# Kernel optimization log

Measured on AMD Instinct MI355X. Metric: run time of the kernel, lower is better.

Reference implementation:

```python
import jax, jax.numpy as jnp
import numpy as np

B, S, DIM, HEADS, HD, FF = 2, 2048, 1024, 16, 64, 4096
PREV, MAX_SEQ, THETA, POS_BIAS_MAX, EPS = 1024, 4096, 10000.0, 2.0, 1e-6


def _freqs_cos_sin():
    inv = 1.0 / THETA ** (np.arange(0, HD, 2)[: HD // 2].astype(np.float32) / HD)
    f = np.outer(np.arange(MAX_SEQ, dtype=np.float32), inv)
    return jnp.asarray(np.cos(f), jnp.float32), jnp.asarray(np.sin(f), jnp.float32)


def setup_inputs():
    key = jax.random.key(0)
    ks = jax.random.split(key, 16)
    lin = lambda k, o, i: 0.02 * jax.random.normal(k, (o, i), jnp.float32)
    cos, sin = _freqs_cos_sin()
    return {
        "x": jax.random.normal(ks[0], (B, S, DIM), jnp.float32),
        "cache_k": jax.random.normal(ks[1], (B, HEADS, PREV, HD), jnp.float32),
        "cache_v": jax.random.normal(ks[2], (B, HEADS, PREV, HD), jnp.float32),
        "cos": cos, "sin": sin,
        "attn_norm_w": jnp.ones((DIM,), jnp.float32),
        "ffn_norm_w": jnp.ones((DIM,), jnp.float32),
        "wq": lin(ks[3], DIM, DIM), "bq": jnp.zeros((DIM,), jnp.float32),
        "wk": lin(ks[4], DIM, DIM), "bk": jnp.zeros((DIM,), jnp.float32),
        "wv": lin(ks[5], DIM, DIM), "bv": jnp.zeros((DIM,), jnp.float32),
        "wo": lin(ks[6], DIM, DIM), "bo": jnp.zeros((DIM,), jnp.float32),
        "w_gate": lin(ks[7], FF, DIM), "b_gate": jnp.zeros((FF,), jnp.float32),
        "w_value": lin(ks[8], FF, DIM), "b_value": jnp.zeros((FF,), jnp.float32),
        "w_proj": lin(ks[9], DIM, FF), "b_proj": jnp.zeros((DIM,), jnp.float32),
        "cache_limit": 3072,
    }


def _rmsnorm(h, w):
    return h * jax.lax.rsqrt(jnp.mean(h * h, axis=-1, keepdims=True) + EPS) * w


def _rope(t, cos, sin):
    # t: [B,H,L,HD]; cos/sin: [L, HD//2]; rotate interleaved pairs (complex mult)
    t2 = t.reshape(t.shape[:-1] + (HD // 2, 2))
    x0, x1 = t2[..., 0], t2[..., 1]
    c = cos[None, None]
    s = sin[None, None]
    out = jnp.stack([x0 * c - x1 * s, x0 * s + x1 * c], axis=-1)
    return out.reshape(t.shape)


def _forward(x, cache_k, cache_v, cos, sin, attn_norm_w, ffn_norm_w, wq, bq, wk, bk, wv, bv, wo, bo, w_gate, b_gate, w_value, b_value, w_proj, b_proj, cache_limit):
    b, s, d = x.shape
    h = _rmsnorm(x, attn_norm_w)
    shape4 = lambda t: t.reshape(b, s, HEADS, HD).transpose(0, 2, 1, 3)  # [B,H,S,HD]
    q = shape4(h @ wq.T + bq)
    k_new = shape4(h @ wk.T + bk)
    v_new = shape4(h @ wv.T + bv)
    k_all = jnp.concatenate([cache_k, k_new], axis=2)
    v_all = jnp.concatenate([cache_v, v_new], axis=2)
    if cache_limit > 0:
        k_all = k_all[:, :, -cache_limit:, :]
        v_all = v_all[:, :, -cache_limit:, :]
    total = k_all.shape[2]
    prev = total - s
    # RoPE: q at absolute positions prev..prev+s-1, keys at 0..total-1 (mod cache len)
    pos_q = (jnp.arange(s) + prev) % MAX_SEQ
    pos_k = jnp.arange(total) % MAX_SEQ
    q = _rope(q, cos[pos_q], sin[pos_q])
    k = _rope(k_all, cos[pos_k], sin[pos_k])
    # linear positional bias + causal mask over the new-token block only
    slope = POS_BIAS_MAX / max(total - 1, 1)
    j = jnp.arange(total, dtype=jnp.float32)[None, :]
    i_abs = (prev + jnp.arange(s, dtype=jnp.float32))[:, None]
    bias = slope * (j - i_abs)  # [s, total]
    causal = (jnp.arange(total)[None, :] - prev) > jnp.arange(s)[:, None]
    mask = jnp.where(causal, -jnp.inf, bias)
    scores = jnp.einsum('bhsd,bhtd->bhst', q, k) / jnp.sqrt(jnp.float32(HD)) + mask
    attn = jax.nn.softmax(scores, axis=-1)
    ctx = jnp.einsum('bhst,bhtd->bhsd', attn, v_all)
    ctx = ctx.transpose(0, 2, 1, 3).reshape(b, s, d)
    x = x + ctx @ wo.T + bo
    h2 = _rmsnorm(x, ffn_norm_w)
    gated = jax.nn.silu(h2 @ w_gate.T + b_gate) * (h2 @ w_value.T + b_value)
    return x + gated @ w_proj.T + b_proj


def reference(x, cache_k, cache_v, cos, sin, attn_norm_w, ffn_norm_w, wq, bq, wk, bk, wv, bv, wo, bo, w_gate, b_gate, w_value, b_value, w_proj, b_proj, cache_limit):
    return _forward(x, cache_k, cache_v, cos, sin, attn_norm_w, ffn_norm_w, wq, bq, wk, bk, wv, bv, wo, bo, w_gate, b_gate, w_value, b_value, w_proj, b_proj, cache_limit)
```

## Files before the change

### kernel.cpp

```cpp
#include <hip/hip_runtime.h>
#include <stdint.h>

typedef unsigned short u16;
typedef unsigned int   u32;
typedef __bf16 bf16x8 __attribute__((ext_vector_type(8)));
typedef float  f32x4  __attribute__((ext_vector_type(4)));
typedef u32    u32x4  __attribute__((ext_vector_type(4)));
typedef u32    u32x2  __attribute__((ext_vector_type(2)));

#define B_SZ  2
#define S_LEN 2048
#define NH    16
#define HD    64
#define DIM   1024
#define FF    4096
#define T_LEN 3072
#define PREV  1024
#define MROWS (B_SZ * S_LEN)
#define LOG2E 1.44269504f

#define MFMA16 __builtin_amdgcn_mfma_f32_16x16x32_bf16

__device__ __forceinline__ u16 f2bf(float f) {
  u32 u = __builtin_bit_cast(u32, f);
  u32 r = u + 0x7FFFu + ((u >> 16) & 1u);
  return (u16)(r >> 16);
}
__device__ __forceinline__ float bf2f(u16 h) {
  u32 u = ((u32)h) << 16;
  return __builtin_bit_cast(float, u);
}
__device__ __forceinline__ u32 cvtpk(float lo, float hi) {
  u32 r;
  asm("v_cvt_pk_bf16_f32 %0, %1, %2" : "=v"(r) : "v"(lo), "v"(hi));
  return r;
}

__device__ __forceinline__ void gl_lds16(const void* g, void* l) {
  __builtin_amdgcn_global_load_lds(
      (const __attribute__((address_space(1))) u32*)g,
      (__attribute__((address_space(3))) u32*)l, 16, 0, 0);
}

#define GFENCE() asm volatile("" ::: "memory")
#define BARF()                         \
  do {                                 \
    GFENCE();                          \
    __builtin_amdgcn_s_barrier();      \
    GFENCE();                          \
  } while (0)

__global__ __launch_bounds__(256) void cvt_kernel(const float* __restrict__ src,
                                                  u16* __restrict__ dst, int n4) {
  int i = blockIdx.x * 256 + threadIdx.x;
  const int stride = gridDim.x * 256;
  for (; i < n4; i += stride) {
    f32x4 v = *(const f32x4*)&src[(long)i * 4];
    u32x2 o;
    o[0] = (u32)f2bf(v[0]) | ((u32)f2bf(v[1]) << 16);
    o[1] = (u32)f2bf(v[2]) | ((u32)f2bf(v[3]) << 16);
    *(u32x2*)&dst[(long)i * 4] = o;
  }
}

__global__ __launch_bounds__(256) void cvt_sw_kernel(const float* __restrict__ src,
                                                     u16* __restrict__ dst, int nunits) {
  int i = blockIdx.x * 256 + threadIdx.x;
  const int stride = gridDim.x * 256;
  for (; i < nunits; i += stride) {
    int row = i >> 7;
    int g = i & 127;
    const float* s = &src[((long)row << 10) + g * 8];
    f32x4 a = *(const f32x4*)s;
    f32x4 b = *(const f32x4*)(s + 4);
    u32x4 o;
    o[0] = (u32)f2bf(a[0]) | ((u32)f2bf(a[1]) << 16);
    o[1] = (u32)f2bf(a[2]) | ((u32)f2bf(a[3]) << 16);
    o[2] = (u32)f2bf(b[0]) | ((u32)f2bf(b[1]) << 16);
    o[3] = (u32)f2bf(b[2]) | ((u32)f2bf(b[3]) << 16);
    const int gp = (g & ~7) | ((g & 7) ^ (row & 7));
    *(u32x4*)&dst[((long)row << 10) + gp * 8] = o;
  }
}

__global__ __launch_bounds__(256) void cvt_ilv_sw_kernel(const float* __restrict__ wg,
                                                         const float* __restrict__ wval,
                                                         u16* __restrict__ dst) {
  int i = blockIdx.x * 256 + threadIdx.x;
  const int stride = gridDim.x * 256;
  for (; i < FF * 128; i += stride) {
    int j = i >> 7;
    int g = i & 127;
    const float* sg = &wg[((long)j << 10) + g * 8];
    const float* sv = &wval[((long)j << 10) + g * 8];
    f32x4 a = *(const f32x4*)sg;
    f32x4 b = *(const f32x4*)(sg + 4);
    u32x4 og;
    og[0] = (u32)f2bf(a[0]) | ((u32)f2bf(a[1]) << 16);
    og[1] = (u32)f2bf(a[2]) | ((u32)f2bf(a[3]) << 16);
    og[2] = (u32)f2bf(b[0]) | ((u32)f2bf(b[1]) << 16);
    og[3] = (u32)f2bf(b[2]) | ((u32)f2bf(b[3]) << 16);
    f32x4 c = *(const f32x4*)sv;
    f32x4 d = *(const f32x4*)(sv + 4);
    u32x4 ov;
    ov[0] = (u32)f2bf(c[0]) | ((u32)f2bf(c[1]) << 16);
    ov[1] = (u32)f2bf(c[2]) | ((u32)f2bf(c[3]) << 16);
    ov[2] = (u32)f2bf(d[0]) | ((u32)f2bf(d[1]) << 16);
    ov[3] = (u32)f2bf(d[2]) | ((u32)f2bf(d[3]) << 16);
    const int rg = 2 * j, rv = 2 * j + 1;
    const int gpg = (g & ~7) | ((g & 7) ^ (rg & 7));
    const int gpv = (g & ~7) | ((g & 7) ^ (rv & 7));
    *(u32x4*)&dst[((long)rg << 10) + gpg * 8] = og;
    *(u32x4*)&dst[((long)rv << 10) + gpv * 8] = ov;
  }
}

__global__ __launch_bounds__(256) void bias_ilv_kernel(const float* __restrict__ bg,
                                                       const float* __restrict__ bval,
                                                       float* __restrict__ dst) {
  int i = blockIdx.x * 256 + threadIdx.x;
  if (i < FF) {
    dst[2 * i] = bg[i];
    dst[2 * i + 1] = bval[i];
  }
}

__global__ __launch_bounds__(256) void rmsnorm_kernel(const float* __restrict__ x,
                                                      const float* __restrict__ w,
                                                      u16* __restrict__ out) {
  const int row = blockIdx.x;
  const int tid = threadIdx.x;
  const long base = (long)row * DIM + tid * 4;
  f32x4 v = *(const f32x4*)&x[base];
  float ss = v[0] * v[0] + v[1] * v[1] + v[2] * v[2] + v[3] * v[3];
#pragma unroll
  for (int d = 1; d <= 32; d <<= 1) ss += __shfl_xor(ss, d, 64);
  __shared__ float red[4];
  if ((tid & 63) == 0) red[tid >> 6] = ss;
  __syncthreads();
  float tot = red[0] + red[1] + red[2] + red[3];
  const float sc = rsqrtf(tot * (1.f / (float)DIM) + 1e-6f);
  f32x4 wv4 = *(const f32x4*)&w[tid * 4];
  u32x2 o;
  o[0] = (u32)f2bf(v[0] * sc * wv4[0]) | ((u32)f2bf(v[1] * sc * wv4[1]) << 16);
  o[1] = (u32)f2bf(v[2] * sc * wv4[2]) | ((u32)f2bf(v[3] * sc * wv4[3]) << 16);
  const int u = tid >> 1, hf = tid & 1;
  const int up = (u & 0x78) | ((u & 7) ^ (row & 7));
  *(u32x2*)&out[(long)row * DIM + up * 8 + hf * 4] = o;
}

template <int EPI>
__global__ __launch_bounds__(512, 2) void gemm256(const u16* __restrict__ A,
                                                  const u16* __restrict__ Bw,
                                                  const float* __restrict__ bias,
                                                  u16* __restrict__ out_bf,
                                                  int N, int K) {
  __shared__ __align__(16) u16 Ab[2][256 * 64];
  __shared__ __align__(16) u16 Bb[2][256 * 64];
  const int tid = threadIdx.x;
  const int lane = tid & 63;
  const int wid = tid >> 6;
  const int wm = wid >> 2, wn = wid & 3;
  const int l15 = lane & 15, lhi = lane >> 4;
  const int c7 = l15 & 7;
  const long m0 = (long)blockIdx.y * 256;
  const long n0 = (long)blockIdx.x * 256;
  const int NT = K >> 6;

  const int srow = tid >> 3;
  const int sunit = (tid & 7) * 8;
  const u16* agp = A + (m0 + srow) * K + sunit;
  const u16* bgp = Bw + (n0 + srow) * K + sunit;
  const int ldst = tid * 8;

  auto stageA = [&](int kt, int b) {
    const int k0 = kt << 6;
    u16* d = &Ab[b][0];
#pragma unroll
    for (int c = 0; c < 4; ++c)
      gl_lds16(agp + (long)(c * 64) * K + k0, d + c * 4096 + ldst);
  };
  auto stageB = [&](int kt, int b) {
    const int k0 = kt << 6;
    u16* d = &Bb[b][0];
#pragma unroll
    for (int c = 0; c < 4; ++c)
      gl_lds16(bgp + (long)(c * 64) * K + k0, d + c * 4096 + ldst);
  };

#define READ_A(MH)                                                               \
  _Pragma("unroll") for (int m_ = 0; m_ < 4; ++m_) {                             \
    _Pragma("unroll") for (int ks_ = 0; ks_ < 2; ++ks_) {                        \
      Afr[MH][m_ * 2 + ks_] =                                                    \
          *(const bf16x8*)&Ac[(wm * 128 + (MH)*64 + m_ * 16 + l15) * 64 +        \
                              (((ks_ * 4 + lhi) ^ c7) * 8)];                     \
    }                                                                            \
  }
#define READ_B(NH)                                                               \
  _Pragma("unroll") for (int n_ = 0; n_ < 2; ++n_) {                             \
    _Pragma("unroll") for (int ks_ = 0; ks_ < 2; ++ks_) {                        \
      Bfr[NH][n_ * 2 + ks_] =                                                    \
          *(const bf16x8*)&Bc[(wn * 64 + (NH)*32 + n_ * 16 + l15) * 64 +         \
                              (((ks_ * 4 + lhi) ^ c7) * 8)];                     \
    }                                                                            \
  }
#define QUAD(MH, NH)                                                             \
  do {                                                                           \
    __builtin_amdgcn_s_setprio(1);                                               \
    _Pragma("unroll") for (int m_ = 0; m_ < 4; ++m_) {                           \
      _Pragma("unroll") for (int n_ = 0; n_ < 2; ++n_) {                         \
        acc[(MH)*4 + m_][(NH)*2 + n_] =                                          \
            MFMA16(Afr[MH][m_ * 2], Bfr[NH][n_ * 2],                             \
                   acc[(MH)*4 + m_][(NH)*2 + n_], 0, 0, 0);                      \
        acc[(MH)*4 + m_][(NH)*2 + n_] =                                          \
            MFMA16(Afr[MH][m_ * 2 + 1], Bfr[NH][n_ * 2 + 1],                     \
                   acc[(MH)*4 + m_][(NH)*2 + n_], 0, 0, 0);                      \
      }                                                                          \
    }                                                                            \
    __builtin_amdgcn_s_setprio(0);                                               \
  } while (0)

  f32x4 acc[8][4] = {};

  stageA(0, 0);
  stageB(0, 0);
  stageA(1, 1);
  stageB(1, 1);
  asm volatile("s_waitcnt vmcnt(8)" ::: "memory");
  __builtin_amdgcn_s_barrier();
  GFENCE();

  for (int kt = 0; kt < NT; ++kt) {
    const int b = kt & 1;
    const u16* Ac = &Ab[b][0];
    const u16* Bc = &Bb[b][0];
    bf16x8 Afr[2][8], Bfr[2][4];
    READ_A(0);
    READ_B(0);
    BARF();
    QUAD(0, 0);
    BARF();
    READ_A(1);
    READ_B(1);
    BARF();
    QUAD(0, 1);
    BARF();
    if (kt + 2 < NT) stageA(kt + 2, b);
    BARF();
    QUAD(1, 0);
    BARF();
    if (kt + 2 < NT) stageB(kt + 2, b);
    BARF();
    QUAD(1, 1);
    if (kt + 1 < NT) {
      if (kt + 2 < NT)
        asm volatile("s_waitcnt vmcnt(8)" ::: "memory");
      else
        asm volatile("s_waitcnt vmcnt(0)" ::: "memory");
      __builtin_amdgcn_s_barrier();
      GFENCE();
    }
  }
#undef READ_A
#undef READ_B
#undef QUAD

#pragma unroll
  for (int mi = 0; mi < 8; ++mi) {
    const long row0 = m0 + wm * 128 + mi * 16 + lhi * 4;
#pragma unroll
    for (int ni = 0; ni < 4; ++ni) {
      const long col = n0 + wn * 64 + ni * 16 + l15;
      const float bb = bias[col];
#pragma unroll
      for (int r = 0; r < 4; ++r) {
        float v = acc[mi][ni][r] + bb;
        if (EPI == 2) {
          float other = __shfl_xor(v, 1, 64);
          if (!(l15 & 1)) {
            float s = v / (1.f + __expf(-v)) * other;
            out_bf[(row0 + r) * (N >> 1) + (col >> 1)] = f2bf(s);
          }
        } else {
          out_bf[(row0 + r) * N + col] = f2bf(v);
        }
      }
    }
  }
}

template <int EPI, int NB>
__global__ __launch_bounds__(256) void gemm_bt(const u16* __restrict__ A,
                                               const u16* __restrict__ Bw,
                                               const float* __restrict__ bias,
                                               const float* __restrict__ resid,
                                               u16* __restrict__ out_bf,
                                               float* __restrict__ out_f,
                                               int N, int K) {
  constexpr int BHALF = NB / 64;
  constexpr int NFR = NB / 32;
  constexpr int LPT = 2 + BHALF;
  __shared__ __align__(16) u16 As[3][128 * 32];
  __shared__ __align__(16) u16 Bs[3][NB * 32];
  const int tid = threadIdx.x;
  const int lane = tid & 63;
  const int wv = tid >> 6;
  const int wr = wv >> 1, wc = wv & 1;
  const long m0 = (long)blockIdx.y * 128;
  const long n0 = (long)blockIdx.x * NB;

  const int arow = tid >> 2;
  const int acol = (tid & 3) << 3;
  const u16* ag = A + (m0 + arow) * K + acol;
  const u16* bg = Bw + (n0 + arow) * K + acol;
  const long hK = (long)64 * K;

  f32x4 acc[4][NFR] = {};
  const int l15 = lane & 15;
  const int lhi = lane >> 4;
  const int aoff0 = (wr * 64 + l15) * 32 + lhi * 8;
  const int boff0 = (wc * (NB / 2) + l15) * 32 + lhi * 8;
  const int nk = K >> 5;

  auto stage = [&](int t, int buf) {
    const int k0 = t << 5;
    gl_lds16(ag + k0, &As[buf][tid * 8]);
    gl_lds16(ag + k0 + hK, &As[buf][2048 + tid * 8]);
    gl_lds16(bg + k0, &Bs[buf][tid * 8]);
    if (BHALF == 2) gl_lds16(bg + k0 + hK, &Bs[buf][2048 + tid * 8]);
  };

  stage(0, 0);
  stage(1, 1);
  asm volatile("s_waitcnt vmcnt(%0)" ::"n"(LPT) : "memory");
  __builtin_amdgcn_s_barrier();
  GFENCE();

  for (int t = 0; t < nk; ++t) {
    const int cb = t % 3;
    if (t + 2 < nk) stage(t + 2, (t + 2) % 3);
    bf16x8 af[4], bfr[NFR];
#pragma unroll
    for (int i = 0; i < 4; ++i) af[i] = *(const bf16x8*)&As[cb][aoff0 + i * 16 * 32];
#pragma unroll
    for (int j = 0; j < NFR; ++j) bfr[j] = *(const bf16x8*)&Bs[cb][boff0 + j * 16 * 32];
    __builtin_amdgcn_s_setprio(1);
#pragma unroll
    for (int i = 0; i < 4; ++i)
#pragma unroll
      for (int j = 0; j < NFR; ++j)
        acc[i][j] = MFMA16(af[i], bfr[j], acc[i][j], 0, 0, 0);
    __builtin_amdgcn_s_setprio(0);
    if (t + 2 < nk) {
      asm volatile("s_waitcnt vmcnt(%0)" ::"n"(LPT) : "memory");
      __builtin_amdgcn_s_barrier();
      GFENCE();
    } else if (t + 1 < nk) {
      asm volatile("s_waitcnt vmcnt(0)" ::: "memory");
      __builtin_amdgcn_s_barrier();
      GFENCE();
    }
  }

#pragma unroll
  for (int i = 0; i < 4; ++i) {
    const long row0 = m0 + wr * 64 + i * 16 + lhi * 4;
#pragma unroll
    for (int j = 0; j < NFR; ++j) {
      const long col = n0 + wc * (NB / 2) + j * 16 + l15;
      const float bb = bias[col];
#pragma unroll
      for (int r = 0; r < 4; ++r) {
        const long idx = (row0 + r) * N + col;
        float v = acc[i][j][r] + bb;
        if (EPI == 0) out_bf[idx] = f2bf(v);
        else          out_f[idx] = resid[idx] + v;
      }
    }
  }
}

__global__ __launch_bounds__(256) void rope_q_kernel(const u16* __restrict__ qkv,
                                                     const float* __restrict__ cosT,
                                                     const float* __restrict__ sinT,
                                                     u16* __restrict__ Q) {
  int idx = blockIdx.x * 256 + threadIdx.x;
  int u = idx & 7;
  int s = (idx >> 3) & (S_LEN - 1);
  int bh = idx >> 14;
  int b = bh >> 4, h = bh & 15;
  int pos = PREV + s;
  const float SC = 0.125f * LOG2E;
  const u16* src = qkv + ((long)(b * S_LEN + s)) * (3 * DIM) + h * HD + u * 8;
  u32x4 d = *(const u32x4*)src;
  f32x4 cv = *(const f32x4*)&cosT[(long)pos * 32 + u * 4];
  f32x4 sv = *(const f32x4*)&sinT[(long)pos * 32 + u * 4];
  u32x4 o;
#pragma unroll
  for (int p = 0; p < 4; ++p) {
    float x0 = bf2f((u16)(d[p] & 0xffff));
    float x1 = bf2f((u16)(d[p] >> 16));
    float y0 = (x0 * cv[p] - x1 * sv[p]) * SC;
    float y1 = (x0 * sv[p] + x1 * cv[p]) * SC;
    o[p] = (u32)f2bf(y0) | ((u32)f2bf(y1) << 16);
  }
  *(u32x4*)&Q[((long)bh * S_LEN + s) * HD + u * 8] = o;
}

__global__ __launch_bounds__(256) void rope_k_kernel(const u16* __restrict__ qkv,
                                                     const float* __restrict__ cache_k,
                                                     const float* __restrict__ cosT,
                                                     const float* __restrict__ sinT,
                                                     u16* __restrict__ Kall) {
  int idx = blockIdx.x * 256 + threadIdx.x;
  int u = idx & 7;
  int t2 = idx >> 3;
  int j = t2 % T_LEN;
  int bh = t2 / T_LEN;
  int b = bh >> 4, h = bh & 15;
  float e[8];
  if (j < PREV) {
    const float* src = cache_k + ((long)bh * PREV + j) * HD + u * 8;
    f32x4 a = *(const f32x4*)src;
    f32x4 c = *(const f32x4*)(src + 4);
    e[0] = a[0]; e[1] = a[1]; e[2] = a[2]; e[3] = a[3];
    e[4] = c[0]; e[5] = c[1]; e[6] = c[2]; e[7] = c[3];
  } else {
    const u16* src = qkv + ((long)(b * S_LEN + (j - PREV))) * (3 * DIM) + DIM + h * HD + u * 8;
    u32x4 d = *(const u32x4*)src;
#pragma unroll
    for (int p = 0; p < 4; ++p) {
      e[2 * p] = bf2f((u16)(d[p] & 0xffff));
      e[2 * p + 1] = bf2f((u16)(d[p] >> 16));
    }
  }
  f32x4 cv = *(const f32x4*)&cosT[(long)j * 32 + u * 4];
  f32x4 sv = *(const f32x4*)&sinT[(long)j * 32 + u * 4];
  u32x4 o;
#pragma unroll
  for (int p = 0; p < 4; ++p) {
    float y0 = e[2 * p] * cv[p] - e[2 * p + 1] * sv[p];
    float y1 = e[2 * p] * sv[p] + e[2 * p + 1] * cv[p];
    o[p] = (u32)f2bf(y0) | ((u32)f2bf(y1) << 16);
  }
  *(u32x4*)&Kall[((long)bh * T_LEN + j) * HD + (u ^ (j & 7)) * 8] = o;
}

__global__ __launch_bounds__(256) void build_vt_kernel(const u16* __restrict__ qkv,
                                                       const float* __restrict__ cache_v,
                                                       u16* __restrict__ Vtg) {
  int idx = blockIdx.x * 256 + threadIdx.x;
  int hd = idx & 63;
  int t2 = idx >> 6;
  int kb = t2 % 384;
  int bh = t2 / 384;
  int b = bh >> 4, h = bh & 15;
  int key0 = kb * 8;
  u16 vals[8];
  if (key0 < PREV) {
#pragma unroll
    for (int i = 0; i < 8; ++i)
      vals[i] = f2bf(cache_v[((long)bh * PREV + key0 + i) * HD + hd]);
  } else {
#pragma unroll
    for (int i = 0; i < 8; ++i)
      vals[i] = qkv[((long)(b * S_LEN + key0 + i - PREV)) * (3 * DIM) + 2 * DIM + h * HD + hd];
  }
  u32x4 o;
#pragma unroll
  for (int p = 0; p < 4; ++p)
    o[p] = (u32)vals[2 * p] | ((u32)vals[2 * p + 1] << 16);
  const int span = kb >> 3;
  const int u = (kb & 7) ^ (hd & 7);
  *(u32x4*)&Vtg[((long)bh * HD + hd) * T_LEN + span * 64 + u * 8] = o;
}

__global__ __launch_bounds__(256, 4) void attn_kernel(const u16* __restrict__ Q,
                                                      const u16* __restrict__ Kg,
                                                      const u16* __restrict__ Vtg,
                                                      u16* __restrict__ ctx, float slope2) {
  __shared__ __align__(16) u16 Ks[2][64 * 64];
  __shared__ __align__(16) u16 Vs[2][64 * 64];
  __shared__ __align__(16) u16 Ps[4][16 * 64];

  const int tid = threadIdx.x;
  const int lane = tid & 63;
  const int wv = tid >> 6;
  const int l15 = lane & 15;
  const int lhi = lane >> 4;
  const int c7 = l15 & 7;
  const int bh = blockIdx.x;
  const int qt = blockIdx.y;
  const int b = bh >> 4, h = bh & 15;
  const int q0 = qt * 64;
  const int nt = (PREV + q0 + 64) >> 6;

  const long qrow = (long)bh * S_LEN + q0 + wv * 16 + l15;
  bf16x8 aq0 = *(const bf16x8*)&Q[qrow * HD + lhi * 8];
  bf16x8 aq1 = *(const bf16x8*)&Q[qrow * HD + 32 + lhi * 8];

  const long kgb = (long)bh * T_LEN * HD;
  const long vgb = (long)bh * HD * T_LEN;
  const int srow = tid >> 3;
  const int sunit = (tid & 7) * 8;

  const u16* kst = Kg + kgb + (long)srow * HD + sunit;
  const u16* vst = Vtg + vgb + (long)srow * T_LEN + sunit;

  gl_lds16(kst, &Ks[0][tid * 8]);
  gl_lds16(kst + 32 * HD, &Ks[0][2048 + tid * 8]);
  gl_lds16(vst, &Vs[0][tid * 8]);
  gl_lds16(vst + (long)32 * T_LEN, &Vs[0][2048 + tid * 8]);
  kst += 64 * HD;
  vst += 64;
  __syncthreads();

  f32x4 o[4] = {};
  f32x4 lrun = {0.f, 0.f, 0.f, 0.f};
  float mrun = -1e30f;
  const int qq = wv * 16 + l15;
  u16* Pw = &Ps[wv][0];

  f32x4 be[4];
#pragma unroll
  for (int jf = 0; jf < 4; ++jf)
#pragma unroll
    for (int r = 0; r < 4; ++r)
      be[jf][r] = slope2 * (float)(jf * 16 + 4 * lhi + r);
  const float bmax = slope2 * 63.f;

  bf16x8 vones;
#pragma unroll
  for (int e = 0; e < 8; ++e) vones[e] = (__bf16)1.0f;

  float ktf = 0.f;
  const float kstep = slope2 * 64.f;

  for (int t = 0; t < nt; ++t) {
    const int cur = t & 1, nxt = cur ^ 1;
    const bool last = (t == nt - 1);
    if (!last) {
      gl_lds16(kst, &Ks[nxt][tid * 8]);
      gl_lds16(kst + 32 * HD, &Ks[nxt][2048 + tid * 8]);
      gl_lds16(vst, &Vs[nxt][tid * 8]);
      gl_lds16(vst + (long)32 * T_LEN, &Vs[nxt][2048 + tid * 8]);
      kst += 64 * HD;
      vst += 64;
    }

    f32x4 sf[4];
    __builtin_amdgcn_s_setprio(1);
#pragma unroll
    for (int jf = 0; jf < 4; ++jf) {
      const int krow = jf * 16 + l15;
      bf16x8 ak0 = *(const bf16x8*)&Ks[cur][krow * 64 + ((lhi ^ c7) * 8)];
      bf16x8 ak1 = *(const bf16x8*)&Ks[cur][krow * 64 + (((4 + lhi) ^ c7) * 8)];
      f32x4 s = {};
      s = MFMA16(ak0, aq0, s, 0, 0, 0);
      s = MFMA16(ak1, aq1, s, 0, 0, 0);
      sf[jf] = s;
    }
    __builtin_amdgcn_s_setprio(0);

    if (last) {
#pragma unroll
      for (int jf = 0; jf < 4; ++jf)
#pragma unroll
        for (int r = 0; r < 4; ++r)
          if (jf * 16 + 4 * lhi + r > qq) sf[jf][r] = -1e30f;
    }

    float h0 = fmaxf(fmaxf(sf[0][0], sf[0][1]), fmaxf(sf[0][2], sf[0][3]));
    float h1 = fmaxf(fmaxf(sf[1][0], sf[1][1]), fmaxf(sf[1][2], sf[1][3]));
    float h2 = fmaxf(fmaxf(sf[2][0], sf[2][1]), fmaxf(sf[2][2], sf[2][3]));
    float h3 = fmaxf(fmaxf(sf[3][0], sf[3][1]), fmaxf(sf[3][2], sf[3][3]));
    float pm = fmaxf(fmaxf(h0, h1), fmaxf(h2, h3));
    pm = fmaxf(pm, __shfl_xor(pm, 16, 64));
    pm = fmaxf(pm, __shfl_xor(pm, 32, 64));
    const float pmax_abs = pm + ktf + bmax;

    if (!__all(pmax_abs - mrun <= 8.f)) {
      const float mnew = fmaxf(mrun, pmax_abs);
      const float scl = exp2f(mrun - mnew);
      mrun = mnew;
#pragma unroll
      for (int r = 0; r < 4; ++r) {
        const float sr = __shfl(scl, 4 * lhi + r, 64);
        lrun[r] *= sr;
#pragma unroll
        for (int hf = 0; hf < 4; ++hf) o[hf][r] *= sr;
      }
    }
    const float meff = mrun - ktf;

#pragma unroll
    for (int jf = 0; jf < 4; ++jf) {
      f32x4 p;
#pragma unroll
      for (int r = 0; r < 4; ++r)
        p[r] = exp2f(sf[jf][r] + (be[jf][r] - meff));
      u32x2 pw2;
      pw2[0] = cvtpk(p[0], p[1]);
      pw2[1] = cvtpk(p[2], p[3]);
      const int u = (2 * jf + (lhi >> 1)) ^ c7;
      *(u32x2*)&Pw[l15 * 64 + u * 8 + (lhi & 1) * 4] = pw2;
    }

    bf16x8 pa0 = *(const bf16x8*)&Pw[l15 * 64 + ((lhi ^ c7) * 8)];
    bf16x8 pa1 = *(const bf16x8*)&Pw[l15 * 64 + (((4 + lhi) ^ c7) * 8)];
    f32x4 psum = {};
    __builtin_amdgcn_s_setprio(1);
    psum = MFMA16(pa0, vones, psum, 0, 0, 0);
    psum = MFMA16(pa1, vones, psum, 0, 0, 0);
#pragma unroll
    for (int hf = 0; hf < 4; ++hf) {
      const int vrow = hf * 16 + l15;
      bf16x8 bv0 = *(const bf16x8*)&Vs[cur][vrow * 64 + ((lhi ^ c7) * 8)];
      bf16x8 bv1 = *(const bf16x8*)&Vs[cur][vrow * 64 + (((4 + lhi) ^ c7) * 8)];
      o[hf] = MFMA16(pa0, bv0, o[hf], 0, 0, 0);
      o[hf] = MFMA16(pa1, bv1, o[hf], 0, 0, 0);
    }
    __builtin_amdgcn_s_setprio(0);
    lrun += psum;

    ktf += kstep;
    if (!last) __syncthreads();
  }

#pragma unroll
  for (int r = 0; r < 4; ++r) {
    const float inv = 1.f / lrun[r];
    const long srow_ = (long)b * S_LEN + q0 + wv * 16 + 4 * lhi + r;
#pragma unroll
    for (int hf = 0; hf < 4; ++hf)
      ctx[srow_ * DIM + h * HD + hf * 16 + l15] = f2bf(o[hf][r] * inv);
  }
}

extern "C" void kernel_launch(void* const* d_in, const int* in_sizes, int n_in,
                              void* d_out, int out_size, void* d_ws, size_t ws_size,
                              hipStream_t stream) {
  (void)in_sizes; (void)n_in; (void)out_size; (void)ws_size;
  const float* x       = (const float*)d_in[0];
  const float* cache_k = (const float*)d_in[1];
  const float* cache_v = (const float*)d_in[2];
  const float* cosT    = (const float*)d_in[3];
  const float* sinT    = (const float*)d_in[4];
  const float* attn_w  = (const float*)d_in[5];
  const float* ffn_w   = (const float*)d_in[6];
  const float* wq      = (const float*)d_in[7];
  const float* bq      = (const float*)d_in[8];
  const float* wk      = (const float*)d_in[9];
  const float* bk      = (const float*)d_in[10];
  const float* wv_     = (const float*)d_in[11];
  const float* bv      = (const float*)d_in[12];
  const float* wo      = (const float*)d_in[13];
  const float* bo      = (const float*)d_in[14];
  const float* wg      = (const float*)d_in[15];
  const float* bg      = (const float*)d_in[16];
  const float* wval    = (const float*)d_in[17];
  const float* bval    = (const float*)d_in[18];
  const float* wp      = (const float*)d_in[19];
  const float* bp      = (const float*)d_in[20];
  float* out = (float*)d_out;

  char* w = (char*)d_ws;
  size_t off = 0;
  auto alloc = [&](size_t bytes) -> char* {
    char* p = w + off;
    off += (bytes + 255) & ~(size_t)255;
    return p;
  };
  u16*   wqkv_bf  = (u16*)alloc((size_t)3 * DIM * DIM * 2);
  u16*   wo_bf    = (u16*)alloc((size_t)DIM * DIM * 2);
  u16*   wgv_bf   = (u16*)alloc((size_t)2 * FF * DIM * 2);
  u16*   wproj_bf = (u16*)alloc((size_t)DIM * FF * 2);
  float* bqkv     = (float*)alloc((size_t)3 * DIM * 4);
  float* bgv      = (float*)alloc((size_t)2 * FF * 4);
  float* x2       = (float*)alloc((size_t)MROWS * DIM * 4);
  char* AR = alloc((size_t)117440512);
  u16* qkv   = (u16*)(AR + 0);
  u16* Qb    = (u16*)(AR + 25165824);
  u16* Kb    = (u16*)(AR + 33554432);
  u16* Vtg   = (u16*)(AR + 46137344);
  u16* h1    = (u16*)(AR + 58720256);
  u16* ctx   = (u16*)(AR + 0);
  u16* h2    = (u16*)(AR + 8388608);
  u16* gated = (u16*)(AR + 16777216);

  cvt_sw_kernel<<<512, 256, 0, stream>>>(wq, wqkv_bf, DIM * DIM / 8);
  cvt_sw_kernel<<<512, 256, 0, stream>>>(wk, wqkv_bf + DIM * DIM, DIM * DIM / 8);
  cvt_sw_kernel<<<512, 256, 0, stream>>>(wv_, wqkv_bf + 2 * DIM * DIM, DIM * DIM / 8);
  cvt_kernel<<<512, 256, 0, stream>>>(wo, wo_bf, DIM * DIM / 4);
  cvt_ilv_sw_kernel<<<1024, 256, 0, stream>>>(wg, wval, wgv_bf);
  cvt_kernel<<<1024, 256, 0, stream>>>(wp, wproj_bf, DIM * FF / 4);
  bias_ilv_kernel<<<16, 256, 0, stream>>>(bg, bval, bgv);
  hipMemcpyAsync(bqkv, bq, DIM * 4, hipMemcpyDeviceToDevice, stream);
  hipMemcpyAsync(bqkv + DIM, bk, DIM * 4, hipMemcpyDeviceToDevice, stream);
  hipMemcpyAsync(bqkv + 2 * DIM, bv, DIM * 4, hipMemcpyDeviceToDevice, stream);

  rmsnorm_kernel<<<MROWS, 256, 0, stream>>>(x, attn_w, h1);
  gemm256<0><<<dim3(12, 16), 512, 0, stream>>>(h1, wqkv_bf, bqkv, qkv, 3 * DIM, DIM);
  rope_q_kernel<<<2048, 256, 0, stream>>>(qkv, cosT, sinT, Qb);
  rope_k_kernel<<<3072, 256, 0, stream>>>(qkv, cache_k, cosT, sinT, Kb);
  build_vt_kernel<<<3072, 256, 0, stream>>>(qkv, cache_v, Vtg);
  attn_kernel<<<dim3(B_SZ * NH, S_LEN / 64), 256, 0, stream>>>(
      Qb, Kb, Vtg, ctx, (2.0f / (float)(T_LEN - 1)) * LOG2E);
  gemm_bt<1, 64><<<dim3(16, 32), 256, 0, stream>>>(ctx, wo_bf, bo, x, nullptr, x2,
                                                   DIM, DIM);
  rmsnorm_kernel<<<MROWS, 256, 0, stream>>>(x2, ffn_w, h2);
  gemm256<2><<<dim3(32, 16), 512, 0, stream>>>(h2, wgv_bf, bgv, gated, 2 * FF, DIM);
  gemm_bt<1, 64><<<dim3(16, 32), 256, 0, stream>>>(gated, wproj_bf, bp, x2, nullptr, out,
                                                   DIM, FF);
}
```

Measured before the change: 383.2 us.

## Pair causal query tiles per block to balance work and share K/V loads

Each attention block now handles two query tiles, p and 31-p, so every block walks a similar number of key tiles under the causal mask. The short tile reuses the K and V tiles already staged in shared memory for the long one, which halves the grid and cuts redundant K/V traffic. The kernel keeps two sets of accumulators and preloads the V fragments into registers, so launch bounds drop to two blocks per SM. That costs occupancy and adds register pressure, and only 512 blocks are launched.

Result: faster. 372.6 us (-2.8%).

```diff
diff --git a/kernel.cpp b/kernel.cpp
--- a/kernel.cpp
+++ b/kernel.cpp
@@ -475,7 +475,7 @@
   *(u32x4*)&Vtg[((long)bh * HD + hd) * T_LEN + span * 64 + u * 8] = o;
 }
 
-__global__ __launch_bounds__(256, 4) void attn_kernel(const u16* __restrict__ Q,
+__global__ __launch_bounds__(256, 2) void attn_kernel(const u16* __restrict__ Q,
                                                       const u16* __restrict__ Kg,
                                                       const u16* __restrict__ Vtg,
                                                       u16* __restrict__ ctx, float slope2) {
@@ -490,14 +490,19 @@
   const int lhi = lane >> 4;
   const int c7 = l15 & 7;
   const int bh = blockIdx.x;
-  const int qt = blockIdx.y;
+  const int p = blockIdx.y;
   const int b = bh >> 4, h = bh & 15;
-  const int q0 = qt * 64;
-  const int nt = (PREV + q0 + 64) >> 6;
-
-  const long qrow = (long)bh * S_LEN + q0 + wv * 16 + l15;
-  bf16x8 aq0 = *(const bf16x8*)&Q[qrow * HD + lhi * 8];
-  bf16x8 aq1 = *(const bf16x8*)&Q[qrow * HD + 32 + lhi * 8];
+  const int qA0 = p * 64;
+  const int qB0 = (31 - p) * 64;
+  const int ntA = 17 + p;
+  const int ntB = 48 - p;
+
+  const long qrowA = (long)bh * S_LEN + qA0 + wv * 16 + l15;
+  const long qrowB = (long)bh * S_LEN + qB0 + wv * 16 + l15;
+  bf16x8 aqA0 = *(const bf16x8*)&Q[qrowA * HD + lhi * 8];
+  bf16x8 aqA1 = *(const bf16x8*)&Q[qrowA * HD + 32 + lhi * 8];
+  bf16x8 aqB0 = *(const bf16x8*)&Q[qrowB * HD + lhi * 8];
+  bf16x8 aqB1 = *(const bf16x8*)&Q[qrowB * HD + 32 + lhi * 8];
 
   const long kgb = (long)bh * T_LEN * HD;
   const long vgb = (long)bh * HD * T_LEN;
@@ -515,9 +520,9 @@
   vst += 64;
   __syncthreads();
 
-  f32x4 o[4] = {};
-  f32x4 lrun = {0.f, 0.f, 0.f, 0.f};
-  float mrun = -1e30f;
+  f32x4 oA[4] = {}, oB[4] = {};
+  f32x4 lrunA = {0.f, 0.f, 0.f, 0.f}, lrunB = {0.f, 0.f, 0.f, 0.f};
+  float mrunA = -1e30f, mrunB = -1e30f;
   const int qq = wv * 16 + l15;
   u16* Pw = &Ps[wv][0];
 
@@ -536,40 +541,15 @@
   float ktf = 0.f;
   const float kstep = slope2 * 64.f;
 
-  for (int t = 0; t < nt; ++t) {
-    const int cur = t & 1, nxt = cur ^ 1;
-    const bool last = (t == nt - 1);
-    if (!last) {
-      gl_lds16(kst, &Ks[nxt][tid * 8]);
-      gl_lds16(kst + 32 * HD, &Ks[nxt][2048 + tid * 8]);
-      gl_lds16(vst, &Vs[nxt][tid * 8]);
-      gl_lds16(vst + (long)32 * T_LEN, &Vs[nxt][2048 + tid * 8]);
-      kst += 64 * HD;
-      vst += 64;
-    }
-
-    f32x4 sf[4];
-    __builtin_amdgcn_s_setprio(1);
-#pragma unroll
-    for (int jf = 0; jf < 4; ++jf) {
-      const int krow = jf * 16 + l15;
-      bf16x8 ak0 = *(const bf16x8*)&Ks[cur][krow * 64 + ((lhi ^ c7) * 8)];
-      bf16x8 ak1 = *(const bf16x8*)&Ks[cur][krow * 64 + (((4 + lhi) ^ c7) * 8)];
-      f32x4 s = {};
-      s = MFMA16(ak0, aq0, s, 0, 0, 0);
-      s = MFMA16(ak1, aq1, s, 0, 0, 0);
-      sf[jf] = s;
-    }
-    __builtin_amdgcn_s_setprio(0);
-
-    if (last) {
+  auto process = [&](f32x4 (&sf)[4], bool maskNow, f32x4 (&o)[4], f32x4& lrun,
+                     float& mrun, bf16x8 (&vf)[8]) {
+    if (maskNow) {
 #pragma unroll
       for (int jf = 0; jf < 4; ++jf)
 #pragma unroll
         for (int r = 0; r < 4; ++r)
           if (jf * 16 + 4 * lhi + r > qq) sf[jf][r] = -1e30f;
     }
-
     float h0 = fmaxf(fmaxf(sf[0][0], sf[0][1]), fmaxf(sf[0][2], sf[0][3]));
     float h1 = fmaxf(fmaxf(sf[1][0], sf[1][1]), fmaxf(sf[1][2], sf[1][3]));
     float h2 = fmaxf(fmaxf(sf[2][0], sf[2][1]), fmaxf(sf[2][2], sf[2][3]));
@@ -595,13 +575,13 @@
 
 #pragma unroll
     for (int jf = 0; jf < 4; ++jf) {
-      f32x4 p;
+      f32x4 pp;
 #pragma unroll
       for (int r = 0; r < 4; ++r)
-        p[r] = exp2f(sf[jf][r] + (be[jf][r] - meff));
+        pp[r] = exp2f(sf[jf][r] + (be[jf][r] - meff));
       u32x2 pw2;
-      pw2[0] = cvtpk(p[0], p[1]);
-      pw2[1] = cvtpk(p[2], p[3]);
+      pw2[0] = cvtpk(pp[0], pp[1]);
+      pw2[1] = cvtpk(pp[2], pp[3]);
       const int u = (2 * jf + (lhi >> 1)) ^ c7;
       *(u32x2*)&Pw[l15 * 64 + u * 8 + (lhi & 1) * 4] = pw2;
     }
@@ -614,26 +594,81 @@
     psum = MFMA16(pa1, vones, psum, 0, 0, 0);
 #pragma unroll
     for (int hf = 0; hf < 4; ++hf) {
-      const int vrow = hf * 16 + l15;
-      bf16x8 bv0 = *(const bf16x8*)&Vs[cur][vrow * 64 + ((lhi ^ c7) * 8)];
-      bf16x8 bv1 = *(const bf16x8*)&Vs[cur][vrow * 64 + (((4 + lhi) ^ c7) * 8)];
-      o[hf] = MFMA16(pa0, bv0, o[hf], 0, 0, 0);
-      o[hf] = MFMA16(pa1, bv1, o[hf], 0, 0, 0);
+      o[hf] = MFMA16(pa0, vf[2 * hf], o[hf], 0, 0, 0);
+      o[hf] = MFMA16(pa1, vf[2 * hf + 1], o[hf], 0, 0, 0);
     }
     __builtin_amdgcn_s_setprio(0);
     lrun += psum;
+  };
+
+  for (int t = 0; t < ntB; ++t) {
+    const int cur = t & 1, nxt = cur ^ 1;
+    const bool lastStage = (t + 1 == ntB);
+    if (!lastStage) {
+      gl_lds16(kst, &Ks[nxt][tid * 8]);
+      gl_lds16(kst + 32 * HD, &Ks[nxt][2048 + tid * 8]);
+      gl_lds16(vst, &Vs[nxt][tid * 8]);
+      gl_lds16(vst + (long)32 * T_LEN, &Vs[nxt][2048 + tid * 8]);
+      kst += 64 * HD;
+      vst += 64;
+    }
+    const bool actA = (t < ntA);
+
+    bf16x8 kf[8];
+#pragma unroll
+    for (int jf = 0; jf < 4; ++jf) {
+      const int krow = jf * 16 + l15;
+      kf[2 * jf] = *(const bf16x8*)&Ks[cur][krow * 64 + ((lhi ^ c7) * 8)];
+      kf[2 * jf + 1] = *(const bf16x8*)&Ks[cur][krow * 64 + (((4 + lhi) ^ c7) * 8)];
+    }
+    bf16x8 vf[8];
+#pragma unroll
+    for (int hf = 0; hf < 4; ++hf) {
+      const int vrow = hf * 16 + l15;
+      vf[2 * hf] = *(const bf16x8*)&Vs[cur][vrow * 64 + ((lhi ^ c7) * 8)];
+      vf[2 * hf + 1] = *(const bf16x8*)&Vs[cur][vrow * 64 + (((4 + lhi) ^ c7) * 8)];
+    }
+
+    f32x4 sB[4], sA[4];
+    __builtin_amdgcn_s_setprio(1);
+#pragma unroll
+    for (int jf = 0; jf < 4; ++jf) {
+      f32x4 s = {};
+      s = MFMA16(kf[2 * jf], aqB0, s, 0, 0, 0);
+      s = MFMA16(kf[2 * jf + 1], aqB1, s, 0, 0, 0);
+      sB[jf] = s;
+    }
+    __builtin_amdgcn_s_setprio(0);
+    if (actA) {
+      __builtin_amdgcn_s_setprio(1);
+#pragma unroll
+      for (int jf = 0; jf < 4; ++jf) {
+        f32x4 s = {};
+        s = MFMA16(kf[2 * jf], aqA0, s, 0, 0, 0);
+        s = MFMA16(kf[2 * jf + 1], aqA1, s, 0, 0, 0);
+        sA[jf] = s;
+      }
+      __builtin_amdgcn_s_setprio(0);
+    }
+
+    process(sB, t == ntB - 1, oB, lrunB, mrunB, vf);
+    if (actA) process(sA, t == ntA - 1, oA, lrunA, mrunA, vf);
 
     ktf += kstep;
-    if (!last) __syncthreads();
+    if (!lastStage) __syncthreads();
   }
 
 #pragma unroll
   for (int r = 0; r < 4; ++r) {
-    const float inv = 1.f / lrun[r];
-    const long srow_ = (long)b * S_LEN + q0 + wv * 16 + 4 * lhi + r;
-#pragma unroll
-    for (int hf = 0; hf < 4; ++hf)
-      ctx[srow_ * DIM + h * HD + hf * 16 + l15] = f2bf(o[hf][r] * inv);
+    const float invA = 1.f / lrunA[r];
+    const float invB = 1.f / lrunB[r];
+    const long rowA = (long)b * S_LEN + qA0 + wv * 16 + 4 * lhi + r;
+    const long rowB = (long)b * S_LEN + qB0 + wv * 16 + 4 * lhi + r;
+#pragma unroll
+    for (int hf = 0; hf < 4; ++hf) {
+      ctx[rowA * DIM + h * HD + hf * 16 + l15] = f2bf(oA[hf][r] * invA);
+      ctx[rowB * DIM + h * HD + hf * 16 + l15] = f2bf(oB[hf][r] * invB);
+    }
   }
 }
 
@@ -704,7 +739,7 @@
   rope_q_kernel<<<2048, 256, 0, stream>>>(qkv, cosT, sinT, Qb);
   rope_k_kernel<<<3072, 256, 0, stream>>>(qkv, cache_k, cosT, sinT, Kb);
   build_vt_kernel<<<3072, 256, 0, stream>>>(qkv, cache_v, Vtg);
-  attn_kernel<<<dim3(B_SZ * NH, S_LEN / 64), 256, 0, stream>>>(
+  attn_kernel<<<dim3(B_SZ * NH, 16), 256, 0, stream>>>(
       Qb, Kb, Vtg, ctx, (2.0f / (float)(T_LEN - 1)) * LOG2E);
   gemm_bt<1, 64><<<dim3(16, 32), 256, 0, stream>>>(ctx, wo_bf, bo, x, nullptr, x2,
                                                    DIM, DIM);
```
